# Kernel tuning notes

Measured on AMD Instinct MI355X. Metric: run time of the kernel, lower is better.

Reference implementation:

```python
import jax, jax.numpy as jnp
import numpy as np

E = 320000   # num edges / messages
N = 10000    # num target nodes (dim_size)
C = 256      # in_channels == out_channels


def setup_inputs() -> dict:
    key = jax.random.key(0)
    k1, k2, k3, k4, k5, k6 = jax.random.split(key, 6)
    s = 1.0 / np.sqrt(C)  # torch Linear default init bound
    return {
        "from_tensor": jax.random.normal(k1, (E, C), dtype=jnp.float32),
        "to_index": jax.random.randint(k2, (E,), 0, N),
        "dim_size": N,
        "W1": jax.random.uniform(k3, (C, C), jnp.float32, -s, s),
        "b1": jax.random.uniform(k4, (C,), jnp.float32, -s, s),
        "W2": jax.random.uniform(k5, (C, C), jnp.float32, -s, s),
        "b2": jax.random.uniform(k6, (C,), jnp.float32, -s, s),
    }


def reference(from_tensor, to_index, dim_size, W1, b1, W2, b2):
    # InterMessage with transform_scatter=True, num_layers=2, reduction='mean':
    # message = MLP(from_tensor); out = scatter_mean(message, to_index, dim_size)
    m = jax.nn.relu(from_tensor @ W1 + b1)          # [E, C]
    m = jax.nn.relu(m @ W2 + b2)                    # [E, C]
    sums = jax.ops.segment_sum(m, to_index, num_segments=dim_size)  # [N, C]
    cnt = jax.ops.segment_sum(jnp.ones((m.shape[0], 1), m.dtype), to_index,
                              num_segments=dim_size)                # [N, 1]
    # scatter-mean: empty segments produce 0 (matches torch_scatter 'mean')
    return jnp.where(cnt > 0, sums / jnp.maximum(cnt, 1.0), 0.0)
```

## Files before the change

kernel.cpp:

```cpp
#include <hip/hip_runtime.h>

#define NUM_E 320000
#define NUM_N 10000

typedef __attribute__((ext_vector_type(8))) short bf16x8;
typedef __attribute__((ext_vector_type(4))) float f32x4;

__device__ __forceinline__ short f2bf(float f) {
  unsigned u = __builtin_bit_cast(unsigned, f);
  u += 0x7FFFu + ((u >> 16) & 1u);
  return (short)(u >> 16);
}

__global__ void prep_w(const float* __restrict__ W1, const float* __restrict__ W2,
                       short* __restrict__ Wp) {
  int gid = blockIdx.x * 256 + threadIdx.x;
  const float* W = (gid & 8192) ? W2 : W1;
  int r = gid & 8191;
  short* dst = Wp + (gid >> 13) * 65536 + r * 8;
  int j = r >> 9;
  int s = (r >> 6) & 7;
  int lane = r & 63;
  int n = j * 16 + (lane & 15);
  int k0 = s * 32 + (lane >> 4) * 8;
  short tmp[8];
#pragma unroll
  for (int e = 0; e < 8; ++e) tmp[e] = f2bf(W[(k0 + e) * 256 + n]);
#pragma unroll
  for (int e = 0; e < 8; ++e) dst[e] = tmp[e];
}

__global__ void hist_k(const int* __restrict__ idx, int* __restrict__ cnt) {
  int e = blockIdx.x * 256 + threadIdx.x;
  if (e < NUM_E) atomicAdd(&cnt[idx[e]], 1);
}

__global__ void scan_k(const int* __restrict__ cnt, int* __restrict__ fill,
                       float* __restrict__ inv) {
  __shared__ int part[256];
  int t = threadIdx.x;
  int base = t * 40;
  int local[40];
  int s = 0;
#pragma unroll
  for (int i = 0; i < 40; ++i) {
    int n = base + i;
    int c = (n < NUM_N) ? cnt[n] : 0;
    local[i] = s;
    s += c;
  }
  part[t] = s;
  __syncthreads();
  for (int off = 1; off < 256; off <<= 1) {
    int tmp = 0;
    if (t >= off) tmp = part[t - off];
    __syncthreads();
    if (t >= off) part[t] += tmp;
    __syncthreads();
  }
  int ebase = (t == 0) ? 0 : part[t - 1];
#pragma unroll
  for (int i = 0; i < 40; ++i) {
    int n = base + i;
    if (n < NUM_N) {
      fill[n] = ebase + local[i];
      int c = cnt[n];
      inv[n] = (c > 0) ? 1.0f / (float)c : 0.0f;
    }
  }
}

__global__ void scatter_k(const int* __restrict__ idx, int* __restrict__ fill,
                          int* __restrict__ sorted) {
  int e = blockIdx.x * 256 + threadIdx.x;
  if (e < NUM_E) {
    int ix = idx[e];
    int pos = atomicAdd(&fill[ix], 1);
    sorted[pos] = e;
  }
}

__global__ __launch_bounds__(256, 2) void fused_mlp_gather(
    const float* __restrict__ X, const int* __restrict__ idx,
    const int* __restrict__ sorted,
    const short* __restrict__ Wp1, const short* __restrict__ Wp2,
    const float* __restrict__ b1, const float* __restrict__ b2,
    const float* __restrict__ inv, float* __restrict__ out) {
  __shared__ __align__(16) float smem[64 * 260];
  short (*Xl)[264] = reinterpret_cast<short(*)[264]>(smem);
  float (*Yout)[260] = reinterpret_cast<float(*)[260]>(smem);
  __shared__ int idxl[64];
  __shared__ int se[64];

  const int tid = threadIdx.x;
  const int wave = tid >> 6;
  const int lane = tid & 63;
  const int q = lane >> 4;
  const int m = lane & 15;
  const int row0 = blockIdx.x * 64;

  if (tid < 64) {
    int e = sorted[row0 + tid];
    se[tid] = e;
    idxl[tid] = idx[e];
  }
  __syncthreads();

  for (int i = tid; i < 64 * 64; i += 256) {
    int r = i >> 6, c4 = i & 63;
    float4 v = reinterpret_cast<const float4*>(X + (size_t)se[r] * 256)[c4];
    unsigned long long packed =
        (unsigned long long)(unsigned short)f2bf(v.x) |
        ((unsigned long long)(unsigned short)f2bf(v.y) << 16) |
        ((unsigned long long)(unsigned short)f2bf(v.z) << 32) |
        ((unsigned long long)(unsigned short)f2bf(v.w) << 48);
    *reinterpret_cast<unsigned long long*>(&Xl[r][c4 * 4]) = packed;
  }
  __syncthreads();

  f32x4 acc[4][4];
#pragma unroll
  for (int mi = 0; mi < 4; ++mi)
#pragma unroll
    for (int nj = 0; nj < 4; ++nj) acc[mi][nj] = (f32x4)0.0f;

#pragma unroll
  for (int s = 0; s < 8; ++s) {
    bf16x8 a[4], b[4];
#pragma unroll
    for (int mi = 0; mi < 4; ++mi)
      a[mi] = *reinterpret_cast<const bf16x8*>(&Xl[mi * 16 + m][s * 32 + q * 8]);
#pragma unroll
    for (int nj = 0; nj < 4; ++nj)
      b[nj] = *reinterpret_cast<const bf16x8*>(
          Wp1 + (size_t)(((wave * 4 + nj) * 8 + s) * 64 + lane) * 8);
#pragma unroll
    for (int mi = 0; mi < 4; ++mi)
#pragma unroll
      for (int nj = 0; nj < 4; ++nj)
        acc[mi][nj] = __builtin_amdgcn_mfma_f32_16x16x32_bf16(a[mi], b[nj],
                                                              acc[mi][nj], 0, 0, 0);
  }
  __syncthreads();

  float bias1[4];
#pragma unroll
  for (int nj = 0; nj < 4; ++nj) bias1[nj] = b1[wave * 64 + nj * 16 + m];
#pragma unroll
  for (int mi = 0; mi < 4; ++mi)
#pragma unroll
    for (int nj = 0; nj < 4; ++nj)
#pragma unroll
      for (int r4 = 0; r4 < 4; ++r4) {
        float v = fmaxf(acc[mi][nj][r4] + bias1[nj], 0.0f);
        Xl[mi * 16 + q * 4 + r4][wave * 64 + nj * 16 + m] = f2bf(v);
      }
  __syncthreads();

#pragma unroll
  for (int mi = 0; mi < 4; ++mi)
#pragma unroll
    for (int nj = 0; nj < 4; ++nj) acc[mi][nj] = (f32x4)0.0f;

#pragma unroll
  for (int s = 0; s < 8; ++s) {
    bf16x8 a[4], b[4];
#pragma unroll
    for (int mi = 0; mi < 4; ++mi)
      a[mi] = *reinterpret_cast<const bf16x8*>(&Xl[mi * 16 + m][s * 32 + q * 8]);
#pragma unroll
    for (int nj = 0; nj < 4; ++nj)
      b[nj] = *reinterpret_cast<const bf16x8*>(
          Wp2 + (size_t)(((wave * 4 + nj) * 8 + s) * 64 + lane) * 8);
#pragma unroll
    for (int mi = 0; mi < 4; ++mi)
#pragma unroll
      for (int nj = 0; nj < 4; ++nj)
        acc[mi][nj] = __builtin_amdgcn_mfma_f32_16x16x32_bf16(a[mi], b[nj],
                                                              acc[mi][nj], 0, 0, 0);
  }
  __syncthreads();

  float bias2[4];
#pragma unroll
  for (int nj = 0; nj < 4; ++nj) bias2[nj] = b2[wave * 64 + nj * 16 + m];
#pragma unroll
  for (int mi = 0; mi < 4; ++mi)
#pragma unroll
    for (int nj = 0; nj < 4; ++nj)
#pragma unroll
      for (int r4 = 0; r4 < 4; ++r4)
        Yout[mi * 16 + q * 4 + r4][wave * 64 + nj * 16 + m] =
            fmaxf(acc[mi][nj][r4] + bias2[nj], 0.0f);
  __syncthreads();

  float run = 0.0f;
  int prev = idxl[0];
  for (int r = 0; r < 64; ++r) {
    int node = idxl[r];
    if (node != prev) {
      if (run != 0.0f) atomicAdd(&out[(size_t)prev * 256 + tid], run * inv[prev]);
      run = 0.0f;
      prev = node;
    }
    run += Yout[r][tid];
  }
  if (run != 0.0f) atomicAdd(&out[(size_t)prev * 256 + tid], run * inv[prev]);
}

extern "C" void kernel_launch(void* const* d_in, const int* in_sizes, int n_in,
                              void* d_out, int out_size, void* d_ws, size_t ws_size,
                              hipStream_t stream) {
  const float* X   = (const float*)d_in[0];
  const int*   idx = (const int*)d_in[1];
  const float* W1  = (const float*)d_in[3];
  const float* b1  = (const float*)d_in[4];
  const float* W2  = (const float*)d_in[5];
  const float* b2  = (const float*)d_in[6];
  float* out = (float*)d_out;

  char* ws = (char*)d_ws;
  short* Wp     = (short*)(ws);
  int*   cnt    = (int*)(ws + 262144);
  int*   fill   = (int*)(ws + 303104);
  float* inv    = (float*)(ws + 344064);
  int*   sorted = (int*)(ws + 385024);

  hipMemsetAsync(out, 0, (size_t)NUM_N * 256 * sizeof(float), stream);
  hipMemsetAsync(cnt, 0, NUM_N * sizeof(int), stream);

  prep_w<<<64, 256, 0, stream>>>(W1, W2, Wp);
  hist_k<<<(NUM_E + 255) / 256, 256, 0, stream>>>(idx, cnt);
  scan_k<<<1, 256, 0, stream>>>(cnt, fill, inv);
  scatter_k<<<(NUM_E + 255) / 256, 256, 0, stream>>>(idx, fill, sorted);
  fused_mlp_gather<<<NUM_E / 64, 256, 0, stream>>>(
      X, idx, sorted, Wp, Wp + 65536, b1, b2, inv, out);
}
```

Baseline: 665.0 us.

## Reduce segments from MFMA registers, shrink LDS, and merge prep kernels

```diff
diff --git a/kernel.cpp b/kernel.cpp
--- a/kernel.cpp
+++ b/kernel.cpp
@@ -12,27 +12,37 @@
   return (short)(u >> 16);
 }
 
-__global__ void prep_w(const float* __restrict__ W1, const float* __restrict__ W2,
-                       short* __restrict__ Wp) {
-  int gid = blockIdx.x * 256 + threadIdx.x;
-  const float* W = (gid & 8192) ? W2 : W1;
-  int r = gid & 8191;
-  short* dst = Wp + (gid >> 13) * 65536 + r * 8;
-  int j = r >> 9;
-  int s = (r >> 6) & 7;
-  int lane = r & 63;
-  int n = j * 16 + (lane & 15);
-  int k0 = s * 32 + (lane >> 4) * 8;
-  short tmp[8];
-#pragma unroll
-  for (int e = 0; e < 8; ++e) tmp[e] = f2bf(W[(k0 + e) * 256 + n]);
-#pragma unroll
-  for (int e = 0; e < 8; ++e) dst[e] = tmp[e];
-}
-
-__global__ void hist_k(const int* __restrict__ idx, int* __restrict__ cnt) {
-  int e = blockIdx.x * 256 + threadIdx.x;
-  if (e < NUM_E) atomicAdd(&cnt[idx[e]], 1);
+__global__ void combo_k(const float* __restrict__ W1, const float* __restrict__ W2,
+                        short* __restrict__ Wp, const int* __restrict__ idx,
+                        int* __restrict__ cnt, float* __restrict__ out) {
+  int b = blockIdx.x;
+  int t = threadIdx.x;
+  if (b < 640) {
+    int base = b * 256 + t;
+#pragma unroll
+    for (int k = 0; k < 4; ++k) {
+      int f4 = base + k * 163840;
+      if (f4 < 640000) reinterpret_cast<float4*>(out)[f4] = make_float4(0, 0, 0, 0);
+    }
+  } else if (b < 1890) {
+    int e = (b - 640) * 256 + t;
+    if (e < NUM_E) atomicAdd(&cnt[idx[e]], 1);
+  } else {
+    int gid = (b - 1890) * 256 + t;
+    const float* W = (gid & 8192) ? W2 : W1;
+    int r = gid & 8191;
+    short* dst = Wp + (gid >> 13) * 65536 + r * 8;
+    int j = r >> 9;
+    int s = (r >> 6) & 7;
+    int lane = r & 63;
+    int n = j * 16 + (lane & 15);
+    int k0 = s * 32 + (lane >> 4) * 8;
+    short tmp[8];
+#pragma unroll
+    for (int e = 0; e < 8; ++e) tmp[e] = f2bf(W[(k0 + e) * 256 + n]);
+#pragma unroll
+    for (int e = 0; e < 8; ++e) dst[e] = tmp[e];
+  }
 }
 
 __global__ void scan_k(const int* __restrict__ cnt, int* __restrict__ fill,
@@ -80,17 +90,18 @@
   }
 }
 
-__global__ __launch_bounds__(256, 2) void fused_mlp_gather(
+__global__ __launch_bounds__(256, 4) void fused_mlp_gather(
     const float* __restrict__ X, const int* __restrict__ idx,
     const int* __restrict__ sorted,
     const short* __restrict__ Wp1, const short* __restrict__ Wp2,
     const float* __restrict__ b1, const float* __restrict__ b2,
     const float* __restrict__ inv, float* __restrict__ out) {
-  __shared__ __align__(16) float smem[64 * 260];
-  short (*Xl)[264] = reinterpret_cast<short(*)[264]>(smem);
-  float (*Yout)[260] = reinterpret_cast<float(*)[260]>(smem);
+  __shared__ __align__(16) short Xl[64][264];
   __shared__ int idxl[64];
   __shared__ int se[64];
+  __shared__ int segLo[64];
+  __shared__ int segN[64];
+  __shared__ int nsegS;
 
   const int tid = threadIdx.x;
   const int wave = tid >> 6;
@@ -118,6 +129,17 @@
   }
   __syncthreads();
 
+  if (wave == 0) {
+    bool flag = (lane == 0) || (idxl[lane] != idxl[lane - 1]);
+    unsigned long long mask = __ballot(flag);
+    if (lane == 0) nsegS = (int)__popcll(mask);
+    if (flag) {
+      int sidx = (int)__popcll(mask & ((1ull << lane) - 1ull));
+      segLo[sidx] = lane;
+      segN[sidx] = idxl[lane];
+    }
+  }
+
   f32x4 acc[4][4];
 #pragma unroll
   for (int mi = 0; mi < 4; ++mi)
@@ -179,7 +201,6 @@
         acc[mi][nj] = __builtin_amdgcn_mfma_f32_16x16x32_bf16(a[mi], b[nj],
                                                               acc[mi][nj], 0, 0, 0);
   }
-  __syncthreads();
 
   float bias2[4];
 #pragma unroll
@@ -190,22 +211,33 @@
     for (int nj = 0; nj < 4; ++nj)
 #pragma unroll
       for (int r4 = 0; r4 < 4; ++r4)
-        Yout[mi * 16 + q * 4 + r4][wave * 64 + nj * 16 + m] =
-            fmaxf(acc[mi][nj][r4] + bias2[nj], 0.0f);
-  __syncthreads();
-
-  float run = 0.0f;
-  int prev = idxl[0];
-  for (int r = 0; r < 64; ++r) {
-    int node = idxl[r];
-    if (node != prev) {
-      if (run != 0.0f) atomicAdd(&out[(size_t)prev * 256 + tid], run * inv[prev]);
-      run = 0.0f;
-      prev = node;
-    }
-    run += Yout[r][tid];
-  }
-  if (run != 0.0f) atomicAdd(&out[(size_t)prev * 256 + tid], run * inv[prev]);
+        acc[mi][nj][r4] = fmaxf(acc[mi][nj][r4] + bias2[nj], 0.0f);
+
+  int nseg = nsegS;
+  for (int s = 0; s < nseg; ++s) {
+    int lo = segLo[s];
+    int hi = (s + 1 < nseg) ? segLo[s + 1] : 64;
+    int node = segN[s];
+    float sum[4] = {0.0f, 0.0f, 0.0f, 0.0f};
+#pragma unroll
+    for (int mi = 0; mi < 4; ++mi)
+#pragma unroll
+      for (int r4 = 0; r4 < 4; ++r4) {
+        int row = mi * 16 + q * 4 + r4;
+        float msk = (row >= lo && row < hi) ? 1.0f : 0.0f;
+#pragma unroll
+        for (int nj = 0; nj < 4; ++nj) sum[nj] = fmaf(msk, acc[mi][nj][r4], sum[nj]);
+      }
+    float scale = inv[node];
+#pragma unroll
+    for (int nj = 0; nj < 4; ++nj) {
+      float v = sum[nj];
+      v += __shfl_xor(v, 16, 64);
+      v += __shfl_xor(v, 32, 64);
+      if (q == 0 && v != 0.0f)
+        atomicAdd(&out[(size_t)node * 256 + wave * 64 + nj * 16 + m], v * scale);
+    }
+  }
 }
 
 extern "C" void kernel_launch(void* const* d_in, const int* in_sizes, int n_in,
@@ -226,11 +258,8 @@
   float* inv    = (float*)(ws + 344064);
   int*   sorted = (int*)(ws + 385024);
 
-  hipMemsetAsync(out, 0, (size_t)NUM_N * 256 * sizeof(float), stream);
   hipMemsetAsync(cnt, 0, NUM_N * sizeof(int), stream);
-
-  prep_w<<<64, 256, 0, stream>>>(W1, W2, Wp);
-  hist_k<<<(NUM_E + 255) / 256, 256, 0, stream>>>(idx, cnt);
+  combo_k<<<1954, 256, 0, stream>>>(W1, W2, Wp, idx, cnt, out);
   scan_k<<<1, 256, 0, stream>>>(cnt, fill, inv);
   scatter_k<<<(NUM_E + 255) / 256, 256, 0, stream>>>(idx, fill, sorted);
   fused_mlp_gather<<<NUM_E / 64, 256, 0, stream>>>(
```

Measured after the change: 586.7 us. 1.13x faster.
